# Kernel tuning notes

Measured on AMD Instinct MI355X. Metric: run time of the kernel, lower is better.

Reference implementation:

```python
import jax, jax.numpy as jnp
import numpy as np

D = 128       # embedding_dim
BC = 64       # block_count
BS = 512      # block_size
K = 6         # main conv kernel size
OV = 2 * BC   # overlap_size
SCALE = 1.0 / np.sqrt(D).astype(np.float32)


def setup_inputs() -> dict:
    key = jax.random.key(0)
    ks = jax.random.split(key, 6)
    B = 8
    x = jax.random.normal(ks[0], (B, BC * BS, D), dtype=jnp.float32)
    w_lw = jax.random.normal(ks[1], (D, 1), dtype=jnp.float32) * 0.05
    b_lw = jnp.zeros((1,), dtype=jnp.float32)
    conv_w = jax.random.normal(ks[2], (D, D, K), dtype=jnp.float32) * 0.05  # (out, in, k)
    conv_b = jnp.zeros((D,), dtype=jnp.float32)
    fusion_w = jax.random.normal(ks[3], (3 * D, D), dtype=jnp.float32) * 0.05
    fusion_b = jnp.zeros((D,), dtype=jnp.float32)
    return {"x": x, "w_lw": w_lw, "b_lw": b_lw, "conv_w": conv_w,
            "conv_b": conv_b, "fusion_w": fusion_w, "fusion_b": fusion_b}


def _prefix_softmax_weighted_sum(x, logits):
    # x: (B, L, D), logits: (B, L) -- faithful replica of the torch scan
    pmax = jax.lax.cummax(logits, axis=1)
    ex = jnp.exp(logits - pmax)                    # (B, L)
    psum = jnp.cumsum(ex, axis=1)                  # (B, L)
    wpre = jnp.cumsum(ex[..., None] * x, axis=1)   # (B, L, D)
    return wpre / psum[..., None]


def _attn(q, k, v):
    # q: (N, 1, D); k, v: (N, S, D)
    s = jnp.einsum('nqd,nkd->nqk', q, k) * SCALE
    return jnp.einsum('nqk,nkd->nqd', jax.nn.softmax(s, axis=-1), v)


def reference(x, w_lw, b_lw, conv_w, conv_b, fusion_w, fusion_b):
    B, L, _ = x.shape  # L == BC * BS, so F.pad in the original is a no-op
    logits = jax.nn.silu(x @ w_lw + b_lw)[..., 0]          # (B, L)
    prefix_x = _prefix_softmax_weighted_sum(x, logits) + x  # (B, L, D)

    # per-block conv1d (kernel 6, padding='same' in torch => pad (2,3))
    blocks = prefix_x.reshape(B * BC, BS, D).transpose(0, 2, 1)  # (N, D, BS)
    conv = jax.lax.conv_general_dilated(
        blocks, conv_w, window_strides=(1,), padding=[(2, 3)],
        dimension_numbers=('NCH', 'OIH', 'NCH')) + conv_b[None, :, None]
    blocks_c = conv.transpose(0, 2, 1)                           # (N, BS, D)
    block_repr = jnp.max(blocks_c, axis=1)[:, None, :]           # (N, 1, D)

    # overlap windows: replicate-pad end by OV//2, slice, gather OV-wide windows
    xov = jnp.pad(prefix_x, ((0, 0), (0, OV // 2), (0, 0)), mode='edge')
    xov = xov[:, BS - OV // 2:, :]                               # (B, (BC-1)*BS + OV, D)
    idx = (jnp.arange(BC) * BS)[:, None] + jnp.arange(OV)[None, :]  # (BC, OV)
    xbo = xov[:, idx, :].reshape(B * BC, OV, D)

    a_s = _attn(block_repr, blocks_c, blocks_c)  # block->self
    a_o = _attn(block_repr, xbo, xbo)            # block->overlap
    fused = jnp.concatenate([a_s, a_o, block_repr], axis=-1)    # (N, 1, 3D)
    out = (fused @ fusion_w + fusion_b).reshape(B, BC, D)
    return (out, out)
```

## Files before the change

kernel.cpp:

```cpp
#include <hip/hip_runtime.h>
#include <hip/hip_bf16.h>

#define NB 8
#define LSEQ 32768
#define DCH 128
#define NCHUNK 1024
#define NSUB 4096
#define NBLK 512
#define PH 520
#define SCALE_F 0.08838834764831845f

typedef __bf16 bf16x8 __attribute__((ext_vector_type(8)));
typedef float f32x4 __attribute__((ext_vector_type(4)));

__device__ __forceinline__ float bf2f(unsigned short u) {
    return __uint_as_float(((unsigned)u) << 16);
}
__device__ __forceinline__ unsigned short f2bf(float f) {
    unsigned u = __float_as_uint(f);
    u += 0x7fffu + ((u >> 16) & 1u);
    return (unsigned short)(u >> 16);
}

__device__ __forceinline__ void async_copy16(const void* gsrc, void* ldst) {
    __builtin_amdgcn_global_load_lds(
        (const __attribute__((address_space(1))) unsigned int*)gsrc,
        (__attribute__((address_space(3))) unsigned int*)ldst, 16, 0, 0);
}

__global__ __launch_bounds__(256) void k_logits2(const float* __restrict__ x,
                                                 const float* __restrict__ w_lw,
                                                 const float* __restrict__ b_lw,
                                                 float* __restrict__ logits,
                                                 float* __restrict__ subM) {
    int chunk = blockIdx.x, t = threadIdx.x;
    int g = t & 15, rs = t >> 4;
    __shared__ float sp[256 * 17];
    __shared__ float red[256];
    float wv[8];
    #pragma unroll
    for (int e = 0; e < 8; ++e) wv[e] = w_lw[g * 8 + e];
    float bb = b_lw[0];
    size_t base = (size_t)chunk * 256 * DCH;
    for (int i = 0; i < 16; ++i) {
        int row = rs * 16 + i;
        float4 a  = *(const float4*)(x + base + (size_t)row * DCH + g * 8);
        float4 b4 = *(const float4*)(x + base + (size_t)row * DCH + g * 8 + 4);
        sp[row * 17 + g] = a.x * wv[0] + a.y * wv[1] + a.z * wv[2] + a.w * wv[3] +
                           b4.x * wv[4] + b4.y * wv[5] + b4.z * wv[6] + b4.w * wv[7];
    }
    __syncthreads();
    float s = bb;
    #pragma unroll
    for (int j = 0; j < 16; ++j) s += sp[t * 17 + j];
    float l = s / (1.f + expf(-s));
    logits[(size_t)chunk * 256 + t] = l;
    red[t] = l;
    __syncthreads();
    for (int off = 32; off >= 1; off >>= 1) {
        if ((t & 63) < off) red[t] = fmaxf(red[t], red[t + off]);
        __syncthreads();
    }
    if ((t & 63) == 0) subM[chunk * 4 + (t >> 6)] = red[t];
}

__global__ __launch_bounds__(64) void k_seed_max2(const float* __restrict__ subM,
                                                  float* __restrict__ seedM) {
    int b = blockIdx.x, lane = threadIdx.x;
    const float* src = subM + b * 512;
    float* dst = seedM + b * 512;
    float v[8];
    float m = -INFINITY;
    #pragma unroll
    for (int j = 0; j < 8; ++j) { v[j] = src[lane * 8 + j]; m = fmaxf(m, v[j]); }
    float incl = m;
    #pragma unroll
    for (int off = 1; off < 64; off <<= 1) {
        float o = __shfl_up(incl, off, 64);
        if (lane >= off) incl = fmaxf(incl, o);
    }
    float ex = __shfl_up(incl, 1, 64);
    if (lane == 0) ex = -INFINITY;
    float run = ex;
    #pragma unroll
    for (int j = 0; j < 8; ++j) { dst[lane * 8 + j] = run; run = fmaxf(run, v[j]); }
}

__global__ __launch_bounds__(256) void k_sums(const float* __restrict__ x,
                                              const float* __restrict__ logits,
                                              const float* __restrict__ seedM,
                                              float* __restrict__ exg,
                                              float* __restrict__ S_w,
                                              float* __restrict__ S_wx) {
    int chunk = blockIdx.x, t = threadIdx.x;
    int g = t & 15, rs = t >> 4;
    __shared__ float llog[256];
    __shared__ float wbuf[256];
    __shared__ float red[256];
    __shared__ float rp[16 * 130];
    llog[t] = logits[(size_t)chunk * 256 + t];
    __syncthreads();
    if (t < 4) {
        float M = seedM[chunk * 4 + t];
        float m = -INFINITY;
        for (int i = 0; i < 64; ++i) {
            float l = llog[t * 64 + i];
            m = fmaxf(m, l);
            wbuf[t * 64 + i] = expf(l - fmaxf(M, m));
        }
    }
    __syncthreads();
    float w_t = wbuf[t];
    exg[(size_t)chunk * 256 + t] = w_t;
    red[t] = w_t;
    __syncthreads();
    for (int off = 32; off >= 1; off >>= 1) {
        if ((t & 63) < off) red[t] += red[t + off];
        __syncthreads();
    }
    if ((t & 63) == 0) S_w[chunk * 4 + (t >> 6)] = red[t];
    float acc[8];
    #pragma unroll
    for (int e = 0; e < 8; ++e) acc[e] = 0.f;
    size_t base = (size_t)chunk * 256 * DCH;
    for (int i = 0; i < 16; ++i) {
        int row = rs * 16 + i;
        float w = wbuf[row];
        float4 a  = *(const float4*)(x + base + (size_t)row * DCH + g * 8);
        float4 b4 = *(const float4*)(x + base + (size_t)row * DCH + g * 8 + 4);
        acc[0] += w * a.x;  acc[1] += w * a.y;  acc[2] += w * a.z;  acc[3] += w * a.w;
        acc[4] += w * b4.x; acc[5] += w * b4.y; acc[6] += w * b4.z; acc[7] += w * b4.w;
    }
    #pragma unroll
    for (int e = 0; e < 8; ++e) rp[rs * 130 + g * 8 + e] = acc[e];
    __syncthreads();
    #pragma unroll
    for (int k = 0; k < 2; ++k) {
        int idx = k * 256 + t;
        int sub = idx >> 7, c = idx & 127;
        float sm = rp[(sub * 4 + 0) * 130 + c] + rp[(sub * 4 + 1) * 130 + c] +
                   rp[(sub * 4 + 2) * 130 + c] + rp[(sub * 4 + 3) * 130 + c];
        S_wx[((size_t)chunk * 4 + sub) * DCH + c] = sm;
    }
}

__global__ __launch_bounds__(64) void k_seed_w(const float* __restrict__ S_w,
                                               float* __restrict__ sS_w) {
    int b = blockIdx.x, lane = threadIdx.x;
    const float* src = S_w + b * 512;
    float* dst = sS_w + b * 512;
    float v[8];
    float tot = 0.f;
    #pragma unroll
    for (int j = 0; j < 8; ++j) { v[j] = src[lane * 8 + j]; tot += v[j]; }
    float incl = tot;
    #pragma unroll
    for (int off = 1; off < 64; off <<= 1) {
        float o = __shfl_up(incl, off, 64);
        if (lane >= off) incl += o;
    }
    float ex = __shfl_up(incl, 1, 64);
    if (lane == 0) ex = 0.f;
    float run = ex;
    #pragma unroll
    for (int j = 0; j < 8; ++j) { dst[lane * 8 + j] = run; run += v[j]; }
}

__global__ __launch_bounds__(256) void k_seed_sums2(const float* __restrict__ S_wx,
                                                    float* __restrict__ sS_wx) {
    int b = blockIdx.x >> 3, cg = blockIdx.x & 7;
    int t = threadIdx.x;
    int cl = t & 15, seg = t >> 4;
    int c = cg * 16 + cl;
    __shared__ float tots[16][17];
    const float* src = S_wx + (size_t)b * 512 * DCH + c;
    float* dst = sS_wx + (size_t)b * 512 * DCH + c;
    int s0 = seg * 32;
    float tot = 0.f;
    for (int j = 0; j < 32; ++j) tot += src[(size_t)(s0 + j) * DCH];
    tots[seg][cl] = tot;
    __syncthreads();
    if (t < 16) {
        float run = 0.f;
        for (int s = 0; s < 16; ++s) { float tmp = tots[s][t]; tots[s][t] = run; run += tmp; }
    }
    __syncthreads();
    float run = tots[seg][cl];
    for (int j = 0; j < 32; ++j) {
        float val = src[(size_t)(s0 + j) * DCH];
        dst[(size_t)(s0 + j) * DCH] = run;
        run += val;
    }
}

__global__ __launch_bounds__(256) void k_init(const float* __restrict__ conv_w,
                                              unsigned short* __restrict__ W3,
                                              unsigned short* __restrict__ P) {
    int n = blockIdx.x, t = threadIdx.x;
    for (int i = t; i < 1024; i += 256) {
        int rr = i >> 7;
        int row = (rr < 2) ? rr : 512 + rr;
        P[(n * PH + row) * DCH + (i & 127)] = 0;
    }
    int idx = n * 256 + t;
    if (idx < 98304) {
        int e  = idx & 7;
        int o  = (idx >> 3) & 127;
        int kc = (idx >> 10) & 3;
        int kt2 = idx >> 12;
        int kt = kt2 >> 1, ks = kt2 & 1;
        int i  = (kt & 1) * 64 + (ks * 4 + kc) * 8 + e;
        int kn = kt >> 1;
        W3[idx] = f2bf(conv_w[(o * 128 + i) * 6 + kn]);
    }
}

__global__ __launch_bounds__(128) void k_apply(const float* __restrict__ x,
                                               const float* __restrict__ exg,
                                               const float* __restrict__ sS_w,
                                               const float* __restrict__ sS_wx,
                                               unsigned short* __restrict__ P) {
    int t = threadIdx.x, w = t >> 6, lane = t & 63;
    int s = blockIdx.x * 2 + w;
    int b = s >> 9, sb = s & 511;
    __shared__ float e2[128];
    e2[t] = exg[(size_t)blockIdx.x * 128 + t];
    float2 axx = *(const float2*)(sS_wx + (size_t)s * DCH + 2 * lane);
    float aex = sS_w[s];
    __syncthreads();
    const float* es = e2 + w * 64;
    int pib0 = sb * 64;
    int n = b * 64 + (pib0 >> 9);
    int row0 = (pib0 & 511) + 2;
    const float* xp = x + ((size_t)b * LSEQ + pib0) * DCH + 2 * lane;
    unsigned short* pp = P + ((size_t)n * PH + row0) * DCH + 2 * lane;
    for (int j = 0; j < 64; ++j) {
        float e = es[j];
        aex += e;
        float2 xv = *(const float2*)xp;
        axx.x += e * xv.x;
        axx.y += e * xv.y;
        float inv = 1.f / aex;
        unsigned pk = ((unsigned)f2bf(axx.y * inv + xv.y) << 16) | f2bf(axx.x * inv + xv.x);
        *(unsigned*)pp = pk;
        xp += DCH;
        pp += DCH;
    }
}

__global__ __launch_bounds__(256) void k_conv(const unsigned short* __restrict__ P,
                                              const unsigned short* __restrict__ W3,
                                              const float* __restrict__ conv_b,
                                              unsigned short* __restrict__ convout) {
    int n = blockIdx.x >> 2;
    int h0 = (blockIdx.x & 3) * 128;
    __shared__ __align__(16) char panel[144 * 256];
    int t = threadIdx.x;
    int wave = t >> 6, lane = t & 63;
    f32x4 acc[4][4] = {};
    const unsigned short* Pn = P + (size_t)n * PH * DCH;
    int wm = (wave >> 1) * 64, wn = (wave & 1) * 64;
    int kchunk = lane >> 4;
    int bcol = wn + (lane & 15);

    bf16x8 breg[2][8];

    auto loadB = [&](int kt, bf16x8* dstB) {
        #pragma unroll
        for (int ks = 0; ks < 2; ++ks)
            #pragma unroll
            for (int ni = 0; ni < 4; ++ni)
                dstB[ks * 4 + ni] = *(const bf16x8*)(
                    W3 + (size_t)((kt * 2 + ks) * 4 + kchunk) * 1024 + (bcol + ni * 16) * 8);
    };

    {
        int c = lane & 15;
        #pragma unroll
        for (int j = 0; j < 9; ++j) {
            int r = j * 16 + wave * 4 + (lane >> 4);
            int gr = h0 + r;
            int grc = min(gr, PH - 1);
            int srcc = (c & 8) | ((c & 7) ^ (gr & 7));
            async_copy16(Pn + (size_t)grc * DCH + srcc * 8,
                         panel + j * 4096 + wave * 1024 + lane * 16);
        }
    }
    loadB(0, breg[0]);
    __syncthreads();

    #pragma unroll
    for (int kt = 0; kt < 12; ++kt) {
        if (kt < 11) loadB(kt + 1, breg[(kt + 1) & 1]);
        int kn = kt >> 1;
        int cb = (kt & 1) * 8;
        #pragma unroll
        for (int ks = 0; ks < 2; ++ks) {
            bf16x8 af[4];
            #pragma unroll
            for (int mi = 0; mi < 4; ++mi) {
                int row = wm + mi * 16 + (lane & 15) + kn;
                int phys = cb + ((ks * 4 + kchunk) ^ ((h0 + row) & 7));
                af[mi] = *(const bf16x8*)(panel + row * 256 + phys * 16);
            }
            #pragma unroll
            for (int mi = 0; mi < 4; ++mi)
                #pragma unroll
                for (int ni = 0; ni < 4; ++ni)
                    acc[mi][ni] = __builtin_amdgcn_mfma_f32_16x16x32_bf16(af[mi],
                                                                          breg[kt & 1][ks * 4 + ni],
                                                                          acc[mi][ni], 0, 0, 0);
        }
    }
    __syncthreads();
    unsigned short* clds = (unsigned short*)panel;
    #pragma unroll
    for (int mi = 0; mi < 4; ++mi)
        #pragma unroll
        for (int ni = 0; ni < 4; ++ni) {
            int col = wn + ni * 16 + (lane & 15);
            float bias = conv_b[col];
            #pragma unroll
            for (int r = 0; r < 4; ++r) {
                int row = wm + mi * 16 + (lane >> 4) * 4 + r;
                clds[row * 136 + col] = f2bf(acc[mi][ni][r] + bias);
            }
        }
    __syncthreads();
    size_t base = (size_t)(n * 512 + h0) * DCH;
    #pragma unroll
    for (int it = 0; it < 8; ++it) {
        int idx = it * 256 + t;
        int row = idx >> 4, g = idx & 15;
        uint4 v = *(const uint4*)(clds + row * 136 + g * 8);
        *(uint4*)(convout + base + (size_t)row * DCH + g * 8) = v;
    }
}

__global__ __launch_bounds__(256) void k_tail(const unsigned short* __restrict__ conv,
                                              const unsigned short* __restrict__ P,
                                              const float* __restrict__ fusion_w,
                                              const float* __restrict__ fusion_b,
                                              float* __restrict__ block_repr,
                                              float* __restrict__ out) {
    int n = blockIdx.x, t = threadIdx.x;
    int g = t & 15, rs = t >> 4;
    int b = n >> 6, c = n & 63;
    __shared__ __align__(16) float sp[512 * 17];
    __shared__ float s[512];
    __shared__ float br[128];
    __shared__ float as_l[128];
    __shared__ float ao_l[128];
    __shared__ float red[128];
    __shared__ int rb[128];
    float* rp = sp;
    const unsigned short* base = conv + (size_t)n * 512 * DCH;

    float m[8];
    #pragma unroll
    for (int e = 0; e < 8; ++e) m[e] = -INFINITY;
    for (int i = 0; i < 32; ++i) {
        int row = i * 16 + rs;
        uint4 v = *(const uint4*)(base + row * DCH + g * 8);
        unsigned vv[4] = {v.x, v.y, v.z, v.w};
        #pragma unroll
        for (int e = 0; e < 4; ++e) {
            m[2 * e]     = fmaxf(m[2 * e],     bf2f((unsigned short)(vv[e] & 0xffff)));
            m[2 * e + 1] = fmaxf(m[2 * e + 1], bf2f((unsigned short)(vv[e] >> 16)));
        }
    }
    #pragma unroll
    for (int e = 0; e < 8; ++e) rp[rs * 130 + g * 8 + e] = m[e];
    __syncthreads();
    if (t < 128) {
        float bm = rp[t];
        #pragma unroll
        for (int r2 = 1; r2 < 16; ++r2) bm = fmaxf(bm, rp[r2 * 130 + t]);
        br[t] = bm;
        block_repr[n * DCH + t] = bm;
    }
    __syncthreads();

    float brv[8];
    #pragma unroll
    for (int e = 0; e < 8; ++e) brv[e] = br[g * 8 + e];
    for (int i = 0; i < 32; ++i) {
        int row = i * 16 + rs;
        uint4 v = *(const uint4*)(base + row * DCH + g * 8);
        unsigned vv[4] = {v.x, v.y, v.z, v.w};
        float p = 0.f;
        #pragma unroll
        for (int e = 0; e < 4; ++e) {
            p += bf2f((unsigned short)(vv[e] & 0xffff)) * brv[2 * e];
            p += bf2f((unsigned short)(vv[e] >> 16))    * brv[2 * e + 1];
        }
        sp[row * 17 + g] = p;
    }
    __syncthreads();
    #pragma unroll
    for (int rr = 0; rr < 2; ++rr) {
        int row = t * 2 + rr;
        float p = 0.f;
        #pragma unroll
        for (int j = 0; j < 16; ++j) p += sp[row * 17 + j];
        s[row] = p * SCALE_F;
    }
    __syncthreads();

    float* redA = sp;
    float mm = fmaxf(s[t], s[t + 256]);
    __syncthreads();
    redA[t] = mm;
    __syncthreads();
    for (int off = 128; off > 0; off >>= 1) {
        if (t < off) redA[t] = fmaxf(redA[t], redA[t + off]);
        __syncthreads();
    }
    float smax = redA[0];
    __syncthreads();
    float e0 = expf(s[t] - smax), e1 = expf(s[t + 256] - smax);
    redA[t] = e0 + e1;
    __syncthreads();
    for (int off = 128; off > 0; off >>= 1) {
        if (t < off) redA[t] += redA[t + off];
        __syncthreads();
    }
    float inv = 1.f / redA[0];
    __syncthreads();
    s[t] = e0 * inv;
    s[t + 256] = e1 * inv;
    __syncthreads();

    float acc[8];
    #pragma unroll
    for (int e = 0; e < 8; ++e) acc[e] = 0.f;
    for (int i = 0; i < 32; ++i) {
        int row = i * 16 + rs;
        float w = s[row];
        uint4 v = *(const uint4*)(base + row * DCH + g * 8);
        unsigned vv[4] = {v.x, v.y, v.z, v.w};
        #pragma unroll
        for (int e = 0; e < 4; ++e) {
            acc[2 * e]     += w * bf2f((unsigned short)(vv[e] & 0xffff));
            acc[2 * e + 1] += w * bf2f((unsigned short)(vv[e] >> 16));
        }
    }
    #pragma unroll
    for (int e = 0; e < 8; ++e) rp[rs * 130 + g * 8 + e] = acc[e];
    __syncthreads();
    if (t < 128) {
        float p = 0.f;
        #pragma unroll
        for (int r2 = 0; r2 < 16; ++r2) p += rp[r2 * 130 + t];
        as_l[t] = p;
    }

    if (t < 128) {
        int pib = (c + 1) * 512 - 64 + t;
        pib = min(pib, LSEQ - 1);
        int n2 = b * 64 + (pib >> 9);
        int row = (pib & 511) + 2;
        rb[t] = (n2 * PH + row) * DCH;
    }
    __syncthreads();
    #pragma unroll
    for (int r = 0; r < 8; ++r) {
        int row = rs * 8 + r;
        uint4 v = *(const uint4*)(P + rb[row] + g * 8);
        unsigned vv[4] = {v.x, v.y, v.z, v.w};
        float p = 0.f;
        #pragma unroll
        for (int e = 0; e < 4; ++e) {
            p += bf2f((unsigned short)(vv[e] & 0xffff)) * brv[2 * e];
            p += bf2f((unsigned short)(vv[e] >> 16))    * brv[2 * e + 1];
        }
        sp[row * 17 + g] = p;
    }
    __syncthreads();
    if (t < 128) {
        float p = 0.f;
        #pragma unroll
        for (int j = 0; j < 16; ++j) p += sp[t * 17 + j];
        s[t] = p * SCALE_F;
        red[t] = s[t];
    }
    __syncthreads();
    for (int off = 64; off > 0; off >>= 1) {
        if (t < off) red[t] = fmaxf(red[t], red[t + off]);
        __syncthreads();
    }
    float smaxB = red[0];
    __syncthreads();
    if (t < 128) {
        float e = expf(s[t] - smaxB);
        s[t] = e;
        red[t] = e;
    }
    __syncthreads();
    for (int off = 64; off > 0; off >>= 1) {
        if (t < off) red[t] += red[t + off];
        __syncthreads();
    }
    float invB = 1.f / red[0];
    __syncthreads();
    if (t < 128) s[t] *= invB;
    __syncthreads();
    float accB[8];
    #pragma unroll
    for (int e = 0; e < 8; ++e) accB[e] = 0.f;
    #pragma unroll
    for (int r = 0; r < 8; ++r) {
        int row = rs * 8 + r;
        float w = s[row];
        uint4 v = *(const uint4*)(P + rb[row] + g * 8);
        unsigned vv[4] = {v.x, v.y, v.z, v.w};
        #pragma unroll
        for (int e = 0; e < 4; ++e) {
            accB[2 * e]     += w * bf2f((unsigned short)(vv[e] & 0xffff));
            accB[2 * e + 1] += w * bf2f((unsigned short)(vv[e] >> 16));
        }
    }
    #pragma unroll
    for (int e = 0; e < 8; ++e) sp[rs * 130 + g * 8 + e] = accB[e];
    __syncthreads();
    if (t < 128) {
        float p = 0.f;
        #pragma unroll
        for (int r2 = 0; r2 < 16; ++r2) p += sp[r2 * 130 + t];
        ao_l[t] = p;
    }
    __syncthreads();

    float* fu = sp + 8320;
    if (t < 128) {
        fu[t] = as_l[t];
        fu[128 + t] = ao_l[t];
        fu[256 + t] = br[t];
    }
    __syncthreads();
    {
        int col = t & 127, h = t >> 7;
        float a2 = (h == 0) ? fusion_b[col] : 0.f;
        for (int j = h * 192; j < h * 192 + 192; ++j)
            a2 += fu[j] * fusion_w[j * DCH + col];
        sp[h * 128 + col] = a2;
    }
    __syncthreads();
    if (t < 128) {
        float v = sp[t] + sp[128 + t];
        out[n * DCH + t] = v;
        out[NB * 64 * DCH + n * DCH + t] = v;
    }
}

extern "C" void kernel_launch(void* const* d_in, const int* in_sizes, int n_in,
                              void* d_out, int out_size, void* d_ws, size_t ws_size,
                              hipStream_t stream) {
    const float* x        = (const float*)d_in[0];
    const float* w_lw     = (const float*)d_in[1];
    const float* b_lw     = (const float*)d_in[2];
    const float* conv_w   = (const float*)d_in[3];
    const float* conv_b   = (const float*)d_in[4];
    const float* fusion_w = (const float*)d_in[5];
    const float* fusion_b = (const float*)d_in[6];
    float* out = (float*)d_out;

    char* ws = (char*)d_ws;
    size_t off = 0;
    auto alloc = [&](size_t bytes) { char* p = ws + off; off += (bytes + 255) & ~(size_t)255; return p; };
    float* logits     = (float*)alloc(NB * LSEQ * 4);
    float* exg        = (float*)alloc(NB * LSEQ * 4);
    float* subM       = (float*)alloc(NSUB * 4);
    float* seedM      = (float*)alloc(NSUB * 4);
    float* S_w        = (float*)alloc(NSUB * 4);
    float* sS_w       = (float*)alloc(NSUB * 4);
    float* S_wx       = (float*)alloc((size_t)NSUB * DCH * 4);
    float* sS_wx      = (float*)alloc((size_t)NSUB * DCH * 4);
    float* block_repr = (float*)alloc(NBLK * DCH * 4);
    unsigned short* W3      = (unsigned short*)alloc(128 * 768 * 2);
    unsigned short* P       = (unsigned short*)alloc((size_t)NBLK * PH * DCH * 2);
    unsigned short* convout = (unsigned short*)alloc((size_t)NBLK * 512 * DCH * 2);

    k_init<<<NBLK, 256, 0, stream>>>(conv_w, W3, P);
    k_logits2<<<NCHUNK, 256, 0, stream>>>(x, w_lw, b_lw, logits, subM);
    k_seed_max2<<<NB, 64, 0, stream>>>(subM, seedM);
    k_sums<<<NCHUNK, 256, 0, stream>>>(x, logits, seedM, exg, S_w, S_wx);
    k_seed_w<<<NB, 64, 0, stream>>>(S_w, sS_w);
    k_seed_sums2<<<NB * 8, 256, 0, stream>>>(S_wx, sS_wx);
    k_apply<<<NSUB / 2, 128, 0, stream>>>(x, exg, sS_w, sS_wx, P);
    k_conv<<<NBLK * 4, 256, 0, stream>>>(P, W3, conv_b, convout);
    k_tail<<<NBLK, 256, 0, stream>>>(convout, P, fusion_w, fusion_b, block_repr, out);
}
```

Measured before the change: 353.4 us.

## Fuse front-end scan kernels into one cooperative kernel with grid syncs

Replaces the six front-end launches (logits, seed max, sums, seed sums, apply) with a single cooperative kernel that uses grid.sync between phases. Per-row logits and exp weights stay in shared memory instead of round-tripping through global buffers, removing the logits and exg global traffic and the launch gaps. It needs all 1024 blocks co-resident, which is checked at runtime with an occupancy query, and falls back to the old multi-kernel path otherwise. Grid-wide barriers add their own cost, and most blocks sit idle during the small serial phases.

Result: no change. 349.9 us (-1.0%).

```diff
diff --git a/kernel.cpp b/kernel.cpp
--- a/kernel.cpp
+++ b/kernel.cpp
@@ -1,5 +1,8 @@
 #include <hip/hip_runtime.h>
 #include <hip/hip_bf16.h>
+#include <hip/hip_cooperative_groups.h>
+
+namespace cg = cooperative_groups;
 
 #define NB 8
 #define LSEQ 32768
@@ -26,6 +29,192 @@
     __builtin_amdgcn_global_load_lds(
         (const __attribute__((address_space(1))) unsigned int*)gsrc,
         (__attribute__((address_space(3))) unsigned int*)ldst, 16, 0, 0);
+}
+
+__global__ __launch_bounds__(256, 4) void k_front(const float* __restrict__ x,
+                                                  const float* __restrict__ w_lw,
+                                                  const float* __restrict__ b_lw,
+                                                  float* __restrict__ subM,
+                                                  float* __restrict__ seedM,
+                                                  float* __restrict__ S_w,
+                                                  float* __restrict__ sS_w,
+                                                  float* __restrict__ S_wx,
+                                                  float* __restrict__ sS_wx,
+                                                  unsigned short* __restrict__ P) {
+    cg::grid_group grid = cg::this_grid();
+    int chunk = blockIdx.x, t = threadIdx.x;
+    int g = t & 15, rs = t >> 4;
+    __shared__ float sp[256 * 17];
+    __shared__ float red[256];
+    __shared__ float wper[256];
+
+    {
+        float wv[8];
+        #pragma unroll
+        for (int e = 0; e < 8; ++e) wv[e] = w_lw[g * 8 + e];
+        float bb = b_lw[0];
+        size_t base = (size_t)chunk * 256 * DCH;
+        for (int i = 0; i < 16; ++i) {
+            int row = rs * 16 + i;
+            float4 a  = *(const float4*)(x + base + (size_t)row * DCH + g * 8);
+            float4 b4 = *(const float4*)(x + base + (size_t)row * DCH + g * 8 + 4);
+            sp[row * 17 + g] = a.x * wv[0] + a.y * wv[1] + a.z * wv[2] + a.w * wv[3] +
+                               b4.x * wv[4] + b4.y * wv[5] + b4.z * wv[6] + b4.w * wv[7];
+        }
+        __syncthreads();
+        float s = bb;
+        #pragma unroll
+        for (int j = 0; j < 16; ++j) s += sp[t * 17 + j];
+        float l = s / (1.f + expf(-s));
+        wper[t] = l;
+        red[t] = l;
+        __syncthreads();
+        for (int off = 32; off >= 1; off >>= 1) {
+            if ((t & 63) < off) red[t] = fmaxf(red[t], red[t + off]);
+            __syncthreads();
+        }
+        if ((t & 63) == 0) subM[chunk * 4 + (t >> 6)] = red[t];
+    }
+    grid.sync();
+
+    if (chunk < 8 && t < 64) {
+        const float* src = subM + chunk * 512;
+        float* dst = seedM + chunk * 512;
+        float v[8];
+        float m = -INFINITY;
+        #pragma unroll
+        for (int j = 0; j < 8; ++j) { v[j] = src[t * 8 + j]; m = fmaxf(m, v[j]); }
+        float incl = m;
+        #pragma unroll
+        for (int off = 1; off < 64; off <<= 1) {
+            float o = __shfl_up(incl, off, 64);
+            if (t >= off) incl = fmaxf(incl, o);
+        }
+        float ex = __shfl_up(incl, 1, 64);
+        if (t == 0) ex = -INFINITY;
+        float run = ex;
+        #pragma unroll
+        for (int j = 0; j < 8; ++j) { dst[t * 8 + j] = run; run = fmaxf(run, v[j]); }
+    }
+    grid.sync();
+
+    {
+        int w = t >> 6, lane = t & 63;
+        float l = wper[t];
+        float M = seedM[chunk * 4 + w];
+        float incl = l;
+        #pragma unroll
+        for (int off = 1; off < 64; off <<= 1) {
+            float o = __shfl_up(incl, off, 64);
+            if (lane >= off) incl = fmaxf(incl, o);
+        }
+        float w_t = expf(l - fmaxf(M, incl));
+        wper[t] = w_t;
+        red[t] = w_t;
+        __syncthreads();
+        for (int off = 32; off >= 1; off >>= 1) {
+            if ((t & 63) < off) red[t] += red[t + off];
+            __syncthreads();
+        }
+        if ((t & 63) == 0) S_w[chunk * 4 + (t >> 6)] = red[t];
+        float acc[8];
+        #pragma unroll
+        for (int e = 0; e < 8; ++e) acc[e] = 0.f;
+        size_t base = (size_t)chunk * 256 * DCH;
+        for (int i = 0; i < 16; ++i) {
+            int row = rs * 16 + i;
+            float ww = wper[row];
+            float4 a  = *(const float4*)(x + base + (size_t)row * DCH + g * 8);
+            float4 b4 = *(const float4*)(x + base + (size_t)row * DCH + g * 8 + 4);
+            acc[0] += ww * a.x;  acc[1] += ww * a.y;  acc[2] += ww * a.z;  acc[3] += ww * a.w;
+            acc[4] += ww * b4.x; acc[5] += ww * b4.y; acc[6] += ww * b4.z; acc[7] += ww * b4.w;
+        }
+        float* rp = sp;
+        #pragma unroll
+        for (int e = 0; e < 8; ++e) rp[rs * 130 + g * 8 + e] = acc[e];
+        __syncthreads();
+        #pragma unroll
+        for (int k = 0; k < 2; ++k) {
+            int idx = k * 256 + t;
+            int sub = idx >> 7, c = idx & 127;
+            float sm = rp[(sub * 4 + 0) * 130 + c] + rp[(sub * 4 + 1) * 130 + c] +
+                       rp[(sub * 4 + 2) * 130 + c] + rp[(sub * 4 + 3) * 130 + c];
+            S_wx[((size_t)chunk * 4 + sub) * DCH + c] = sm;
+        }
+    }
+    grid.sync();
+
+    if (chunk < 8) {
+        if (t < 64) {
+            const float* src = S_w + chunk * 512;
+            float* dst = sS_w + chunk * 512;
+            float v[8];
+            float tot = 0.f;
+            #pragma unroll
+            for (int j = 0; j < 8; ++j) { v[j] = src[t * 8 + j]; tot += v[j]; }
+            float incl = tot;
+            #pragma unroll
+            for (int off = 1; off < 64; off <<= 1) {
+                float o = __shfl_up(incl, off, 64);
+                if (t >= off) incl += o;
+            }
+            float ex = __shfl_up(incl, 1, 64);
+            if (t == 0) ex = 0.f;
+            float run = ex;
+            #pragma unroll
+            for (int j = 0; j < 8; ++j) { dst[t * 8 + j] = run; run += v[j]; }
+        }
+    } else if (chunk < 72) {
+        int b = (chunk - 8) >> 3, cgx = (chunk - 8) & 7;
+        int cl = t & 15, seg = t >> 4;
+        int c = cgx * 16 + cl;
+        float* tots = sp;
+        const float* src = S_wx + (size_t)b * 512 * DCH + c;
+        float* dst = sS_wx + (size_t)b * 512 * DCH + c;
+        int s0 = seg * 32;
+        float tot = 0.f;
+        for (int j = 0; j < 32; ++j) tot += src[(size_t)(s0 + j) * DCH];
+        tots[seg * 17 + cl] = tot;
+        __syncthreads();
+        if (t < 16) {
+            float run = 0.f;
+            for (int s2 = 0; s2 < 16; ++s2) { float tmp = tots[s2 * 17 + t]; tots[s2 * 17 + t] = run; run += tmp; }
+        }
+        __syncthreads();
+        float run = tots[seg * 17 + cl];
+        for (int j = 0; j < 32; ++j) {
+            float val = src[(size_t)(s0 + j) * DCH];
+            dst[(size_t)(s0 + j) * DCH] = run;
+            run += val;
+        }
+    }
+    grid.sync();
+
+    {
+        int w = t >> 6, lane = t & 63;
+        int s = chunk * 4 + w;
+        int b = s >> 9, sb = s & 511;
+        float2 axx = *(const float2*)(sS_wx + (size_t)s * DCH + 2 * lane);
+        float aex = sS_w[s];
+        const float* es = wper + w * 64;
+        int pib0 = sb * 64;
+        int n = b * 64 + (pib0 >> 9);
+        int row0 = (pib0 & 511) + 2;
+        const float* xp = x + ((size_t)b * LSEQ + pib0) * DCH + 2 * lane;
+        unsigned short* pp = P + ((size_t)n * PH + row0) * DCH + 2 * lane;
+        for (int j = 0; j < 64; ++j) {
+            float e = es[j];
+            aex += e;
+            float2 xv = *(const float2*)xp;
+            axx.x += e * xv.x;
+            axx.y += e * xv.y;
+            float inv = 1.f / aex;
+            unsigned pk = ((unsigned)f2bf(axx.y * inv + xv.y) << 16) | f2bf(axx.x * inv + xv.x);
+            *(unsigned*)pp = pk;
+            xp += DCH;
+            pp += DCH;
+        }
+    }
 }
 
 __global__ __launch_bounds__(256) void k_logits2(const float* __restrict__ x,
@@ -168,10 +357,10 @@
 
 __global__ __launch_bounds__(256) void k_seed_sums2(const float* __restrict__ S_wx,
                                                     float* __restrict__ sS_wx) {
-    int b = blockIdx.x >> 3, cg = blockIdx.x & 7;
+    int b = blockIdx.x >> 3, cgx = blockIdx.x & 7;
     int t = threadIdx.x;
     int cl = t & 15, seg = t >> 4;
-    int c = cg * 16 + cl;
+    int c = cgx * 16 + cl;
     __shared__ float tots[16][17];
     const float* src = S_wx + (size_t)b * 512 * DCH + c;
     float* dst = sS_wx + (size_t)b * 512 * DCH + c;
@@ -190,28 +379,6 @@
         float val = src[(size_t)(s0 + j) * DCH];
         dst[(size_t)(s0 + j) * DCH] = run;
         run += val;
-    }
-}
-
-__global__ __launch_bounds__(256) void k_init(const float* __restrict__ conv_w,
-                                              unsigned short* __restrict__ W3,
-                                              unsigned short* __restrict__ P) {
-    int n = blockIdx.x, t = threadIdx.x;
-    for (int i = t; i < 1024; i += 256) {
-        int rr = i >> 7;
-        int row = (rr < 2) ? rr : 512 + rr;
-        P[(n * PH + row) * DCH + (i & 127)] = 0;
-    }
-    int idx = n * 256 + t;
-    if (idx < 98304) {
-        int e  = idx & 7;
-        int o  = (idx >> 3) & 127;
-        int kc = (idx >> 10) & 3;
-        int kt2 = idx >> 12;
-        int kt = kt2 >> 1, ks = kt2 & 1;
-        int i  = (kt & 1) * 64 + (ks * 4 + kc) * 8 + e;
-        int kn = kt >> 1;
-        W3[idx] = f2bf(conv_w[(o * 128 + i) * 6 + kn]);
     }
 }
 
@@ -245,6 +412,28 @@
         *(unsigned*)pp = pk;
         xp += DCH;
         pp += DCH;
+    }
+}
+
+__global__ __launch_bounds__(256) void k_init(const float* __restrict__ conv_w,
+                                              unsigned short* __restrict__ W3,
+                                              unsigned short* __restrict__ P) {
+    int n = blockIdx.x, t = threadIdx.x;
+    for (int i = t; i < 1024; i += 256) {
+        int rr = i >> 7;
+        int row = (rr < 2) ? rr : 512 + rr;
+        P[(n * PH + row) * DCH + (i & 127)] = 0;
+    }
+    int idx = n * 256 + t;
+    if (idx < 98304) {
+        int e  = idx & 7;
+        int o  = (idx >> 3) & 127;
+        int kc = (idx >> 10) & 3;
+        int kt2 = idx >> 12;
+        int kt = kt2 >> 1, ks = kt2 & 1;
+        int i  = (kt & 1) * 64 + (ks * 4 + kc) * 8 + e;
+        int kn = kt >> 1;
+        W3[idx] = f2bf(conv_w[(o * 128 + i) * 6 + kn]);
     }
 }
 
@@ -582,12 +771,41 @@
     unsigned short* convout = (unsigned short*)alloc((size_t)NBLK * 512 * DCH * 2);
 
     k_init<<<NBLK, 256, 0, stream>>>(conv_w, W3, P);
-    k_logits2<<<NCHUNK, 256, 0, stream>>>(x, w_lw, b_lw, logits, subM);
-    k_seed_max2<<<NB, 64, 0, stream>>>(subM, seedM);
-    k_sums<<<NCHUNK, 256, 0, stream>>>(x, logits, seedM, exg, S_w, S_wx);
-    k_seed_w<<<NB, 64, 0, stream>>>(S_w, sS_w);
-    k_seed_sums2<<<NB * 8, 256, 0, stream>>>(S_wx, sS_wx);
-    k_apply<<<NSUB / 2, 128, 0, stream>>>(x, exg, sS_w, sS_wx, P);
+
+    static int coop_ok = -1;
+    if (coop_ok < 0) {
+        int dev = 0, ncu = 0, maxb = 0;
+        coop_ok = 0;
+        if (hipGetDevice(&dev) == hipSuccess &&
+            hipDeviceGetAttribute(&ncu, hipDeviceAttributeMultiprocessorCount, dev) == hipSuccess &&
+            hipOccupancyMaxActiveBlocksPerMultiprocessor(&maxb, (const void*)k_front, 256, 0) == hipSuccess) {
+            if ((long)maxb * ncu >= NCHUNK) coop_ok = 1;
+        }
+        (void)hipGetLastError();
+    }
+
+    bool coop_done = false;
+    if (coop_ok == 1) {
+        void* cargs[] = {(void*)&x, (void*)&w_lw, (void*)&b_lw, (void*)&subM, (void*)&seedM,
+                         (void*)&S_w, (void*)&sS_w, (void*)&S_wx, (void*)&sS_wx, (void*)&P};
+        hipError_t ce = hipLaunchCooperativeKernel((const void*)k_front, dim3(NCHUNK), dim3(256),
+                                                   cargs, 0, stream);
+        if (ce == hipSuccess) {
+            coop_done = true;
+        } else {
+            (void)hipGetLastError();
+            coop_ok = 0;
+        }
+    }
+    if (!coop_done) {
+        k_logits2<<<NCHUNK, 256, 0, stream>>>(x, w_lw, b_lw, logits, subM);
+        k_seed_max2<<<NB, 64, 0, stream>>>(subM, seedM);
+        k_sums<<<NCHUNK, 256, 0, stream>>>(x, logits, seedM, exg, S_w, S_wx);
+        k_seed_w<<<NB, 64, 0, stream>>>(S_w, sS_w);
+        k_seed_sums2<<<NB * 8, 256, 0, stream>>>(S_wx, sS_wx);
+        k_apply<<<NSUB / 2, 128, 0, stream>>>(x, exg, sS_w, sS_wx, P);
+    }
+
     k_conv<<<NBLK * 4, 256, 0, stream>>>(P, W3, conv_b, convout);
     k_tail<<<NBLK, 256, 0, stream>>>(convout, P, fusion_w, fusion_b, block_repr, out);
 }
```
